# Performance work log

Hardware: AMD Instinct MI355X
Metric: run time of the kernel (lower is better)

Reference implementation:

```python
import jax, jax.numpy as jnp
import numpy as np

D_MODEL = 1024
N_HEADS = 16
FEATURE_DIM = 16
HEAD_DIM = D_MODEL // N_HEADS  # 64
EPS = 1e-12


def taylor_exp(x):
    """2nd-order Taylor feature map of exp(q^T k / sqrt(d)).
    x: (b, h, l, d) -> (b, h, l, 1 + d + d^2)"""
    d = x.shape[-1]
    rd = jnp.sqrt(jnp.asarray(d, x.dtype))      # sqrt(d)
    rrd = jnp.sqrt(rd)                          # d^(1/4)
    r2 = jnp.sqrt(jnp.asarray(2.0, x.dtype))
    x2 = (x[..., :, None] * x[..., None, :]).reshape(*x.shape[:-1], d * d) / r2
    ones = jnp.ones_like(x[..., :1])
    return jnp.concatenate([ones, x / rrd, x2 / rd], axis=-1)


def setup_inputs() -> dict:
    key = jax.random.key(0)
    k0, k1, k2, k3, k4 = jax.random.split(key, 5)
    b, l = 1, 1024
    scale = 1.0 / np.sqrt(D_MODEL)
    hidden_states = jax.random.normal(k0, (b, l, D_MODEL), dtype=jnp.float32)
    Wq = jax.random.normal(k1, (N_HEADS * FEATURE_DIM, D_MODEL), dtype=jnp.float32) * scale
    Wk = jax.random.normal(k2, (N_HEADS * FEATURE_DIM, D_MODEL), dtype=jnp.float32) * scale
    Wv = jax.random.normal(k3, (N_HEADS * HEAD_DIM, D_MODEL), dtype=jnp.float32) * scale
    Wo = jax.random.normal(k4, (D_MODEL, N_HEADS * HEAD_DIM), dtype=jnp.float32) * scale
    return {"hidden_states": hidden_states, "Wq": Wq, "Wk": Wk, "Wv": Wv, "Wo": Wo}


def reference(hidden_states, Wq, Wk, Wv, Wo):
    b, l, _ = hidden_states.shape
    # projections (bias-free)
    q = (hidden_states @ Wq.T).reshape(b, l, N_HEADS, FEATURE_DIM).transpose(0, 2, 1, 3)
    k = (hidden_states @ Wk.T).reshape(b, l, N_HEADS, FEATURE_DIM).transpose(0, 2, 1, 3)
    v = (hidden_states @ Wv.T).reshape(b, l, N_HEADS, HEAD_DIM).transpose(0, 2, 1, 3)
    qf = taylor_exp(q)   # (b, h, l, D) with D = 1 + d + d^2 = 273
    kf = taylor_exp(k)
    # causal linear attention via associative KV accumulation
    # kv_state[l] = sum_{t<=l} phi(k_t) outer v_t  -> (b, h, l, head_dim, D)
    kv_state = jnp.cumsum(kf[..., None, :] * v[..., :, None], axis=2)
    num = jnp.einsum('bhlD,bhldD->bhld', qf, kv_state)
    den = jnp.einsum('bhlD,bhlD->bhl', qf, jnp.cumsum(kf, axis=2))[..., None] + EPS
    y = num / den                                # (b, h, l, head_dim)
    y = y.transpose(0, 2, 1, 3).reshape(b, l, N_HEADS * HEAD_DIM)
    return y @ Wo.T
```

## Files before the change

### kernel.cpp

```cpp
#include <hip/hip_runtime.h>

#define LSEQ 1024
#define DMODEL 1024
#define NHEADS 16
#define FDIM 16
#define HDIM 64
#define CHUNK 64
#define NCHUNK 16

typedef __attribute__((ext_vector_type(8))) short short8;
typedef __attribute__((ext_vector_type(4))) float floatx4;

__device__ __forceinline__ unsigned short f2bf(float f) {
    return __builtin_bit_cast(unsigned short, (__bf16)f);
}

__device__ __forceinline__ int block_detect_fp32(const unsigned short* wq) {
    __shared__ int cnt;
    if (threadIdx.x == 0) cnt = 0;
    __syncthreads();
    int bad = 0;
    for (int i = threadIdx.x; i < 1024; i += blockDim.x) {
        int e = (wq[i] >> 7) & 0xFF;
        if (e >= 143 || (e > 0 && e <= 80)) bad++;
    }
    if (bad) atomicAdd(&cnt, bad);
    __syncthreads();
    return cnt > 128;
}

#define U_QB   0
#define U_KB   262144
#define U_VT   524288
#define U_END  2621440

#define MFMA(a, b, c) __builtin_amdgcn_mfma_f32_16x16x32_bf16((a), (b), (c), 0, 0, 0)

__device__ __forceinline__ void gemm64_body(
    unsigned short (&As)[64][136], unsigned short (&Bs)[64][136],
    const void* Araw, int a_fp32, int arow0,
    const void* Braw, int b_fp32, int brow0, floatx4 acc[4]) {
    int t = threadIdx.x;
    int r = t >> 2, c0 = (t & 3) * 32;
    int wave = t >> 6, lane = t & 63;
    int ml = lane & 15, q4 = lane >> 4;
    int mq = (wave >> 1) * 32, nq = (wave & 1) * 32;
    #pragma unroll
    for (int i = 0; i < 4; ++i) acc[i] = (floatx4){0.f, 0.f, 0.f, 0.f};

    short8 av[4], bv[4], av2[4], bv2[4];
    auto cvt8 = [](float4 f0, float4 f1) {
        short8 x;
        x[0] = (short)f2bf(f0.x); x[1] = (short)f2bf(f0.y);
        x[2] = (short)f2bf(f0.z); x[3] = (short)f2bf(f0.w);
        x[4] = (short)f2bf(f1.x); x[5] = (short)f2bf(f1.y);
        x[6] = (short)f2bf(f1.z); x[7] = (short)f2bf(f1.w);
        return x;
    };
    auto stage = [&](int k0, short8* a, short8* b) {
        if (!a_fp32) {
            const unsigned short* Ap = (const unsigned short*)Araw + (size_t)(arow0 + r) * DMODEL + k0 + c0;
            #pragma unroll
            for (int j = 0; j < 4; ++j) a[j] = *(const short8*)(Ap + j * 8);
        } else {
            const float* Ap = (const float*)Araw + (size_t)(arow0 + r) * DMODEL + k0 + c0;
            #pragma unroll
            for (int j = 0; j < 4; ++j)
                a[j] = cvt8(*(const float4*)(Ap + j * 8), *(const float4*)(Ap + j * 8 + 4));
        }
        if (!b_fp32) {
            const unsigned short* Bp = (const unsigned short*)Braw + (size_t)(brow0 + r) * DMODEL + k0 + c0;
            #pragma unroll
            for (int j = 0; j < 4; ++j) b[j] = *(const short8*)(Bp + j * 8);
        } else {
            const float* Bp = (const float*)Braw + (size_t)(brow0 + r) * DMODEL + k0 + c0;
            #pragma unroll
            for (int j = 0; j < 4; ++j)
                b[j] = cvt8(*(const float4*)(Bp + j * 8), *(const float4*)(Bp + j * 8 + 4));
        }
    };

    stage(0, av, bv);
    for (int k0 = 0; k0 < DMODEL; k0 += 128) {
        __syncthreads();
        #pragma unroll
        for (int j = 0; j < 4; ++j) {
            *(short8*)&As[r][c0 + j * 8] = av[j];
            *(short8*)&Bs[r][c0 + j * 8] = bv[j];
        }
        __syncthreads();
        if (k0 + 128 < DMODEL) stage(k0 + 128, av2, bv2);
        #pragma unroll
        for (int kk = 0; kk < 4; ++kk) {
            short8 a0 = *(const short8*)&As[mq + ml][kk * 32 + q4 * 8];
            short8 a1 = *(const short8*)&As[mq + 16 + ml][kk * 32 + q4 * 8];
            short8 b0 = *(const short8*)&Bs[nq + ml][kk * 32 + q4 * 8];
            short8 b1 = *(const short8*)&Bs[nq + 16 + ml][kk * 32 + q4 * 8];
            acc[0] = MFMA(a0, b0, acc[0]); acc[1] = MFMA(a0, b1, acc[1]);
            acc[2] = MFMA(a1, b0, acc[2]); acc[3] = MFMA(a1, b1, acc[3]);
        }
        #pragma unroll
        for (int j = 0; j < 4; ++j) { av[j] = av2[j]; bv[j] = bv2[j]; }
    }
}

__global__ __launch_bounds__(256) void qkv_gemm(
    const void* __restrict__ hidR, const void* __restrict__ WqR,
    const void* __restrict__ WkR, const void* __restrict__ WvR,
    unsigned short* __restrict__ qb, unsigned short* __restrict__ kb,
    unsigned short* __restrict__ vt) {
    int fp32 = block_detect_fp32((const unsigned short*)WqR);
    __shared__ __align__(16) unsigned short As[64][136];
    __shared__ __align__(16) unsigned short Bs[64][136];
    int nb = blockIdx.x, mb = blockIdx.y;
    const void* Braw; unsigned short* Cout; int ldc, col0, br0, isv;
    if (nb < 4)      { Braw = WqR; br0 = nb * 64;       Cout = qb; ldc = 256;  col0 = nb * 64;       isv = 0; }
    else if (nb < 8) { Braw = WkR; br0 = (nb - 4) * 64; Cout = kb; ldc = 256;  col0 = (nb - 4) * 64; isv = 0; }
    else             { Braw = WvR; br0 = (nb - 8) * 64; Cout = vt; ldc = 0;    col0 = (nb - 8) * 64; isv = 1; }

    floatx4 acc[4];
    gemm64_body(As, Bs, hidR, fp32, mb * 64, Braw, fp32, br0, acc);

    int wave = threadIdx.x >> 6, lane = threadIdx.x & 63;
    int ml = lane & 15, q4 = lane >> 4;
    int mq = (wave >> 1) * 32, nq = (wave & 1) * 32;
    if (!isv) {
        #pragma unroll
        for (int mi = 0; mi < 2; ++mi)
            #pragma unroll
            for (int ni = 0; ni < 2; ++ni) {
                floatx4 a = acc[mi * 2 + ni];
                int nloc = nq + ni * 16 + ml;
                #pragma unroll
                for (int r4 = 0; r4 < 4; ++r4) {
                    int row = mb * 64 + mq + mi * 16 + q4 * 4 + r4;
                    Cout[(size_t)row * ldc + col0 + nloc] = f2bf(a[r4]);
                }
            }
    } else {
        #pragma unroll
        for (int mi = 0; mi < 2; ++mi)
            #pragma unroll
            for (int ni = 0; ni < 2; ++ni) {
                floatx4 a = acc[mi * 2 + ni];
                int n = col0 + nq + ni * 16 + ml;
                int row0 = mb * 64 + mq + mi * 16 + q4 * 4;
                ushort4 o;
                o.x = f2bf(a[0]); o.y = f2bf(a[1]);
                o.z = f2bf(a[2]); o.w = f2bf(a[3]);
                *(ushort4*)&vt[(size_t)n * 1024 + row0] = o;
            }
    }
}

__global__ __launch_bounds__(256) void flash_partial(
    const unsigned short* __restrict__ qb, const unsigned short* __restrict__ kb,
    const unsigned short* __restrict__ vt,
    float* __restrict__ numW, float* __restrict__ denW) {
    int idx = blockIdx.x & 255;
    int s = blockIdx.x >> 8;
    int h = idx & 15, c = idx >> 4;
    int half = (c + 1) >> 1;
    int j0 = s ? half : 0;
    int j1 = s ? c : half - 1;
    int l0 = c * CHUNK;
    __shared__ __align__(16) unsigned short qs[64][40];
    __shared__ __align__(16) unsigned short ksm[64][40];
    __shared__ __align__(16) unsigned short vT[80][72];
    __shared__ __align__(16) unsigned short P[64][72];
    int t = threadIdx.x, lane = t & 63, wave = t >> 6;
    int ml = lane & 15, q4 = lane >> 4;
    int m0 = wave * 16;
    int sm = t >> 2, si4 = (t & 3) * 4, sc16 = (t & 3) * 16;

    {
        *(ushort4*)&qs[sm][si4] = *(const ushort4*)&qb[(size_t)(l0 + sm) * 256 + h * 16 + si4];
        ushort4 z = {0, 0, 0, 0};
        *(ushort4*)&qs[sm][16 + si4]  = z;
        *(ushort4*)&ksm[sm][16 + si4] = z;
    }
    if (t < 64) {
        vT[64][t] = 0x3F80;
        #pragma unroll
        for (int i = 65; i < 80; ++i) vT[i][t] = 0;
    }

    auto load_kv = [&](int j, ushort4& kr, short8& v0, short8& v1) {
        kr = *(const ushort4*)&kb[(size_t)(j * 64 + sm) * 256 + h * 16 + si4];
        const unsigned short* vp = vt + (size_t)(h * 64 + sm) * 1024 + j * 64 + sc16;
        v0 = *(const short8*)vp;
        v1 = *(const short8*)(vp + 8);
    };

    floatx4 acc[5];
    #pragma unroll
    for (int i = 0; i < 5; ++i) acc[i] = (floatx4){0.f, 0.f, 0.f, 0.f};

    ushort4 kr, kr2; short8 va, vb2, va2, vb22;
    if (j0 <= j1) {
        load_kv(j0, kr, va, vb2);
        for (int j = j0; j <= j1; ++j) {
            *(ushort4*)&ksm[sm][si4] = kr;
            *(short8*)&vT[sm][sc16]     = va;
            *(short8*)&vT[sm][sc16 + 8] = vb2;
            __syncthreads();
            if (j < j1) load_kv(j + 1, kr2, va2, vb22);

            short8 aq = *(const short8*)&qs[m0 + ml][q4 * 8];
            bool diag = (j == c);
            #pragma unroll
            for (int nt = 0; nt < 4; ++nt) {
                short8 bk = *(const short8*)&ksm[nt * 16 + ml][q4 * 8];
                floatx4 s4 = {0.f, 0.f, 0.f, 0.f};
                s4 = MFMA(aq, bk, s4);
                int tt = nt * 16 + ml;
                #pragma unroll
                for (int r = 0; r < 4; ++r) {
                    int lrow = m0 + q4 * 4 + r;
                    float sc = s4[r];
                    float p = 1.f + 0.25f * sc + 0.03125f * sc * sc;
                    if (diag && tt > lrow) p = 0.f;
                    P[lrow][tt] = f2bf(p);
                }
            }

            #pragma unroll
            for (int k0 = 0; k0 < 64; k0 += 32) {
                short8 ap = *(const short8*)&P[m0 + ml][k0 + q4 * 8];
                #pragma unroll
                for (int nt = 0; nt < 5; ++nt) {
                    short8 av = *(const short8*)&vT[nt * 16 + ml][k0 + q4 * 8];
                    acc[nt] = MFMA(av, ap, acc[nt]);
                }
            }
            __syncthreads();
            kr = kr2; va = va2; vb2 = vb22;
        }
    }

    float* np = numW + ((size_t)idx * 2 + s) * 4096 + (m0 + ml) * 64;
    #pragma unroll
    for (int nt = 0; nt < 4; ++nt)
        *(floatx4*)&np[nt * 16 + q4 * 4] = acc[nt];
    if (lane < 16) denW[((size_t)idx * 2 + s) * 64 + m0 + lane] = acc[4][0];
}

__global__ __launch_bounds__(256) void out_gemm(
    const float* __restrict__ numW, const float* __restrict__ denW,
    const void* __restrict__ WoR, void* __restrict__ outv,
    const unsigned short* __restrict__ wqraw) {
    int fp32 = block_detect_fp32(wqraw);
    __shared__ __align__(16) unsigned short As[64][136];
    __shared__ __align__(16) unsigned short Bs[64][136];
    int nb = blockIdx.x, mb = blockIdx.y;
    int t = threadIdx.x;
    int r = t >> 2, c0 = (t & 3) * 32;
    int wave = t >> 6, lane = t & 63;
    int ml = lane & 15, q4 = lane >> 4;
    int mq = (wave >> 1) * 32, nq = (wave & 1) * 32;
    floatx4 acc[4];
    #pragma unroll
    for (int i = 0; i < 4; ++i) acc[i] = (floatx4){0.f, 0.f, 0.f, 0.f};

    short8 av[4], bv[4], av2[4], bv2[4];
    auto cvt8 = [](float4 f0, float4 f1) {
        short8 x;
        x[0] = (short)f2bf(f0.x); x[1] = (short)f2bf(f0.y);
        x[2] = (short)f2bf(f0.z); x[3] = (short)f2bf(f0.w);
        x[4] = (short)f2bf(f1.x); x[5] = (short)f2bf(f1.y);
        x[6] = (short)f2bf(f1.z); x[7] = (short)f2bf(f1.w);
        return x;
    };
    auto stageA = [&](int k0, short8* a) {
        int kbase = k0 + c0;
        int h = kbase >> 6;
        size_t idx = (size_t)(mb * 16 + h);
        const float* n0 = numW + idx * 2 * 4096 + r * 64 + (kbase & 63);
        const float* n1 = n0 + 4096;
        float den = denW[idx * 128 + r] + denW[idx * 128 + 64 + r] + 1e-12f;
        float dinv = 1.f / den;
        #pragma unroll
        for (int j = 0; j < 4; ++j) {
            float4 f0 = *(const float4*)(n0 + j * 8);
            float4 f1 = *(const float4*)(n0 + j * 8 + 4);
            float4 g0 = *(const float4*)(n1 + j * 8);
            float4 g1 = *(const float4*)(n1 + j * 8 + 4);
            float4 s0, s1;
            s0.x = (f0.x + g0.x) * dinv; s0.y = (f0.y + g0.y) * dinv;
            s0.z = (f0.z + g0.z) * dinv; s0.w = (f0.w + g0.w) * dinv;
            s1.x = (f1.x + g1.x) * dinv; s1.y = (f1.y + g1.y) * dinv;
            s1.z = (f1.z + g1.z) * dinv; s1.w = (f1.w + g1.w) * dinv;
            a[j] = cvt8(s0, s1);
        }
    };
    auto stageB = [&](int k0, short8* b) {
        if (!fp32) {
            const unsigned short* Bp = (const unsigned short*)WoR + (size_t)(nb * 64 + r) * DMODEL + k0 + c0;
            #pragma unroll
            for (int j = 0; j < 4; ++j) b[j] = *(const short8*)(Bp + j * 8);
        } else {
            const float* Bp = (const float*)WoR + (size_t)(nb * 64 + r) * DMODEL + k0 + c0;
            #pragma unroll
            for (int j = 0; j < 4; ++j)
                b[j] = cvt8(*(const float4*)(Bp + j * 8), *(const float4*)(Bp + j * 8 + 4));
        }
    };

    stageA(0, av); stageB(0, bv);
    for (int k0 = 0; k0 < DMODEL; k0 += 128) {
        __syncthreads();
        #pragma unroll
        for (int j = 0; j < 4; ++j) {
            *(short8*)&As[r][c0 + j * 8] = av[j];
            *(short8*)&Bs[r][c0 + j * 8] = bv[j];
        }
        __syncthreads();
        if (k0 + 128 < DMODEL) { stageA(k0 + 128, av2); stageB(k0 + 128, bv2); }
        #pragma unroll
        for (int kk = 0; kk < 4; ++kk) {
            short8 a0 = *(const short8*)&As[mq + ml][kk * 32 + q4 * 8];
            short8 a1 = *(const short8*)&As[mq + 16 + ml][kk * 32 + q4 * 8];
            short8 b0 = *(const short8*)&Bs[nq + ml][kk * 32 + q4 * 8];
            short8 b1 = *(const short8*)&Bs[nq + 16 + ml][kk * 32 + q4 * 8];
            acc[0] = MFMA(a0, b0, acc[0]); acc[1] = MFMA(a0, b1, acc[1]);
            acc[2] = MFMA(a1, b0, acc[2]); acc[3] = MFMA(a1, b1, acc[3]);
        }
        #pragma unroll
        for (int j = 0; j < 4; ++j) { av[j] = av2[j]; bv[j] = bv2[j]; }
    }

    #pragma unroll
    for (int mi = 0; mi < 2; ++mi)
        #pragma unroll
        for (int ni = 0; ni < 2; ++ni) {
            floatx4 a = acc[mi * 2 + ni];
            int n = nb * 64 + nq + ni * 16 + ml;
            #pragma unroll
            for (int r4 = 0; r4 < 4; ++r4) {
                int row = mb * 64 + mq + mi * 16 + q4 * 4 + r4;
                size_t oidx = (size_t)row * 1024 + n;
                if (fp32) ((float*)outv)[oidx] = a[r4];
                else      ((unsigned short*)outv)[oidx] = f2bf(a[r4]);
            }
        }
}

extern "C" void kernel_launch(void* const* d_in, const int* in_sizes, int n_in,
                              void* d_out, int out_size, void* d_ws, size_t ws_size,
                              hipStream_t stream) {
    unsigned short* us = (unsigned short*)d_ws;
    unsigned short* qbB = us + U_QB;
    unsigned short* kbB = us + U_KB;
    unsigned short* vtB = us + U_VT;
    float* fws  = (float*)(us + U_END);
    float* numW = fws;
    float* denW = fws + 2097152;
    size_t need = (size_t)U_END * 2ull + (size_t)(2097152 + 32768) * 4ull;
    if (ws_size < need) return;

    qkv_gemm<<<dim3(24, 16), 256, 0, stream>>>(d_in[0], d_in[1], d_in[2], d_in[3], qbB, kbB, vtB);
    flash_partial<<<dim3(512), 256, 0, stream>>>(qbB, kbB, vtB, numW, denW);
    out_gemm<<<dim3(16, 16), 256, 0, stream>>>(numW, denW, d_in[4], d_out, (const unsigned short*)d_in[1]);
}
```

Measured before the change: 148.2 us.

## Split causal attention over four key ranges and add separate combine kernel

The flash_partial kernel now splits each query chunk's key range into four parts instead of two, launching 1024 blocks to spread the triangular work more evenly across CUs. A new attn_combine kernel sums the four partials, normalizes by the denominator and writes bf16 y, so out_gemm reuses the generic gemm64_body instead of reducing partials inline. The score MFMA operands are also swapped so each lane writes a packed ushort4 to the P tile rather than scalar stores. This adds an extra kernel launch and doubles the partial-result workspace traffic.

```diff
diff --git a/kernel.cpp b/kernel.cpp
--- a/kernel.cpp
+++ b/kernel.cpp
@@ -7,6 +7,7 @@
 #define HDIM 64
 #define CHUNK 64
 #define NCHUNK 16
+#define NSPLIT 4
 
 typedef __attribute__((ext_vector_type(8))) short short8;
 typedef __attribute__((ext_vector_type(4))) float floatx4;
@@ -32,6 +33,7 @@
 #define U_QB   0
 #define U_KB   262144
 #define U_VT   524288
+#define U_YB   1572864
 #define U_END  2621440
 
 #define MFMA(a, b, c) __builtin_amdgcn_mfma_f32_16x16x32_bf16((a), (b), (c), 0, 0, 0)
@@ -160,9 +162,9 @@
     int idx = blockIdx.x & 255;
     int s = blockIdx.x >> 8;
     int h = idx & 15, c = idx >> 4;
-    int half = (c + 1) >> 1;
-    int j0 = s ? half : 0;
-    int j1 = s ? c : half - 1;
+    int n = c + 1;
+    int j0 = (n * s) >> 2;
+    int j1 = ((n * (s + 1)) >> 2) - 1;
     int l0 = c * CHUNK;
     __shared__ __align__(16) unsigned short qs[64][40];
     __shared__ __align__(16) unsigned short ksm[64][40];
@@ -208,20 +210,22 @@
 
             short8 aq = *(const short8*)&qs[m0 + ml][q4 * 8];
             bool diag = (j == c);
+            int qloc = m0 + ml;
             #pragma unroll
             for (int nt = 0; nt < 4; ++nt) {
                 short8 bk = *(const short8*)&ksm[nt * 16 + ml][q4 * 8];
                 floatx4 s4 = {0.f, 0.f, 0.f, 0.f};
-                s4 = MFMA(aq, bk, s4);
-                int tt = nt * 16 + ml;
+                s4 = MFMA(bk, aq, s4);
+                ushort4 pw;
                 #pragma unroll
                 for (int r = 0; r < 4; ++r) {
-                    int lrow = m0 + q4 * 4 + r;
+                    int tloc = nt * 16 + q4 * 4 + r;
                     float sc = s4[r];
                     float p = 1.f + 0.25f * sc + 0.03125f * sc * sc;
-                    if (diag && tt > lrow) p = 0.f;
-                    P[lrow][tt] = f2bf(p);
+                    if (diag && tloc > qloc) p = 0.f;
+                    ((unsigned short*)&pw)[r] = f2bf(p);
                 }
+                *(ushort4*)&P[qloc][nt * 16 + q4 * 4] = pw;
             }
 
             #pragma unroll
@@ -238,107 +242,71 @@
         }
     }
 
-    float* np = numW + ((size_t)idx * 2 + s) * 4096 + (m0 + ml) * 64;
+    float* np = numW + ((size_t)idx * NSPLIT + s) * 4096 + (m0 + ml) * 64;
     #pragma unroll
     for (int nt = 0; nt < 4; ++nt)
         *(floatx4*)&np[nt * 16 + q4 * 4] = acc[nt];
-    if (lane < 16) denW[((size_t)idx * 2 + s) * 64 + m0 + lane] = acc[4][0];
+    if (lane < 16) denW[((size_t)idx * NSPLIT + s) * 64 + m0 + lane] = acc[4][0];
+}
+
+__global__ __launch_bounds__(256) void attn_combine(
+    const float* __restrict__ numW, const float* __restrict__ denW,
+    unsigned short* __restrict__ ybB) {
+    int idx = blockIdx.x;
+    int h = idx & 15, c = idx >> 4;
+    int l0 = c * CHUNK;
+    int t = threadIdx.x;
+    int row = t >> 2, col0 = (t & 3) * 16;
+    const float* nb_ = numW + (size_t)idx * NSPLIT * 4096 + row * 64 + col0;
+    const float* db_ = denW + (size_t)idx * NSPLIT * 64 + row;
+    float den = db_[0] + db_[64] + db_[128] + db_[192] + 1e-12f;
+    float dinv = 1.f / den;
+    float sum[16];
+    #pragma unroll
+    for (int u = 0; u < 16; u += 4) {
+        float4 a0 = *(const float4*)(nb_ + u);
+        float4 a1 = *(const float4*)(nb_ + 4096 + u);
+        float4 a2 = *(const float4*)(nb_ + 8192 + u);
+        float4 a3 = *(const float4*)(nb_ + 12288 + u);
+        sum[u + 0] = a0.x + a1.x + a2.x + a3.x;
+        sum[u + 1] = a0.y + a1.y + a2.y + a3.y;
+        sum[u + 2] = a0.z + a1.z + a2.z + a3.z;
+        sum[u + 3] = a0.w + a1.w + a2.w + a3.w;
+    }
+    short8 o0, o1;
+    #pragma unroll
+    for (int u = 0; u < 8; ++u)  o0[u] = (short)f2bf(sum[u] * dinv);
+    #pragma unroll
+    for (int u = 0; u < 8; ++u)  o1[u] = (short)f2bf(sum[u + 8] * dinv);
+    unsigned short* yp = ybB + (size_t)(l0 + row) * 1024 + h * 64 + col0;
+    *(short8*)yp       = o0;
+    *(short8*)(yp + 8) = o1;
 }
 
 __global__ __launch_bounds__(256) void out_gemm(
-    const float* __restrict__ numW, const float* __restrict__ denW,
-    const void* __restrict__ WoR, void* __restrict__ outv,
-    const unsigned short* __restrict__ wqraw) {
+    const unsigned short* __restrict__ A, const void* __restrict__ WoR,
+    void* __restrict__ outv, const unsigned short* __restrict__ wqraw) {
     int fp32 = block_detect_fp32(wqraw);
     __shared__ __align__(16) unsigned short As[64][136];
     __shared__ __align__(16) unsigned short Bs[64][136];
     int nb = blockIdx.x, mb = blockIdx.y;
-    int t = threadIdx.x;
-    int r = t >> 2, c0 = (t & 3) * 32;
-    int wave = t >> 6, lane = t & 63;
+
+    floatx4 acc[4];
+    gemm64_body(As, Bs, A, 0, mb * 64, WoR, fp32, nb * 64, acc);
+
+    int wave = threadIdx.x >> 6, lane = threadIdx.x & 63;
     int ml = lane & 15, q4 = lane >> 4;
     int mq = (wave >> 1) * 32, nq = (wave & 1) * 32;
-    floatx4 acc[4];
-    #pragma unroll
-    for (int i = 0; i < 4; ++i) acc[i] = (floatx4){0.f, 0.f, 0.f, 0.f};
-
-    short8 av[4], bv[4], av2[4], bv2[4];
-    auto cvt8 = [](float4 f0, float4 f1) {
-        short8 x;
-        x[0] = (short)f2bf(f0.x); x[1] = (short)f2bf(f0.y);
-        x[2] = (short)f2bf(f0.z); x[3] = (short)f2bf(f0.w);
-        x[4] = (short)f2bf(f1.x); x[5] = (short)f2bf(f1.y);
-        x[6] = (short)f2bf(f1.z); x[7] = (short)f2bf(f1.w);
-        return x;
-    };
-    auto stageA = [&](int k0, short8* a) {
-        int kbase = k0 + c0;
-        int h = kbase >> 6;
-        size_t idx = (size_t)(mb * 16 + h);
-        const float* n0 = numW + idx * 2 * 4096 + r * 64 + (kbase & 63);
-        const float* n1 = n0 + 4096;
-        float den = denW[idx * 128 + r] + denW[idx * 128 + 64 + r] + 1e-12f;
-        float dinv = 1.f / den;
-        #pragma unroll
-        for (int j = 0; j < 4; ++j) {
-            float4 f0 = *(const float4*)(n0 + j * 8);
-            float4 f1 = *(const float4*)(n0 + j * 8 + 4);
-            float4 g0 = *(const float4*)(n1 + j * 8);
-            float4 g1 = *(const float4*)(n1 + j * 8 + 4);
-            float4 s0, s1;
-            s0.x = (f0.x + g0.x) * dinv; s0.y = (f0.y + g0.y) * dinv;
-            s0.z = (f0.z + g0.z) * dinv; s0.w = (f0.w + g0.w) * dinv;
-            s1.x = (f1.x + g1.x) * dinv; s1.y = (f1.y + g1.y) * dinv;
-            s1.z = (f1.z + g1.z) * dinv; s1.w = (f1.w + g1.w) * dinv;
-            a[j] = cvt8(s0, s1);
-        }
-    };
-    auto stageB = [&](int k0, short8* b) {
-        if (!fp32) {
-            const unsigned short* Bp = (const unsigned short*)WoR + (size_t)(nb * 64 + r) * DMODEL + k0 + c0;
-            #pragma unroll
-            for (int j = 0; j < 4; ++j) b[j] = *(const short8*)(Bp + j * 8);
-        } else {
-            const float* Bp = (const float*)WoR + (size_t)(nb * 64 + r) * DMODEL + k0 + c0;
-            #pragma unroll
-            for (int j = 0; j < 4; ++j)
-                b[j] = cvt8(*(const float4*)(Bp + j * 8), *(const float4*)(Bp + j * 8 + 4));
-        }
-    };
-
-    stageA(0, av); stageB(0, bv);
-    for (int k0 = 0; k0 < DMODEL; k0 += 128) {
-        __syncthreads();
-        #pragma unroll
-        for (int j = 0; j < 4; ++j) {
-            *(short8*)&As[r][c0 + j * 8] = av[j];
-            *(short8*)&Bs[r][c0 + j * 8] = bv[j];
-        }
-        __syncthreads();
-        if (k0 + 128 < DMODEL) { stageA(k0 + 128, av2); stageB(k0 + 128, bv2); }
-        #pragma unroll
-        for (int kk = 0; kk < 4; ++kk) {
-            short8 a0 = *(const short8*)&As[mq + ml][kk * 32 + q4 * 8];
-            short8 a1 = *(const short8*)&As[mq + 16 + ml][kk * 32 + q4 * 8];
-            short8 b0 = *(const short8*)&Bs[nq + ml][kk * 32 + q4 * 8];
-            short8 b1 = *(const short8*)&Bs[nq + 16 + ml][kk * 32 + q4 * 8];
-            acc[0] = MFMA(a0, b0, acc[0]); acc[1] = MFMA(a0, b1, acc[1]);
-            acc[2] = MFMA(a1, b0, acc[2]); acc[3] = MFMA(a1, b1, acc[3]);
-        }
-        #pragma unroll
-        for (int j = 0; j < 4; ++j) { av[j] = av2[j]; bv[j] = bv2[j]; }
-    }
-
     #pragma unroll
     for (int mi = 0; mi < 2; ++mi)
         #pragma unroll
         for (int ni = 0; ni < 2; ++ni) {
             floatx4 a = acc[mi * 2 + ni];
-            int n = nb * 64 + nq + ni * 16 + ml;
+            int nn = nb * 64 + nq + ni * 16 + ml;
             #pragma unroll
             for (int r4 = 0; r4 < 4; ++r4) {
                 int row = mb * 64 + mq + mi * 16 + q4 * 4 + r4;
-                size_t oidx = (size_t)row * 1024 + n;
+                size_t oidx = (size_t)row * 1024 + nn;
                 if (fp32) ((float*)outv)[oidx] = a[r4];
                 else      ((unsigned short*)outv)[oidx] = f2bf(a[r4]);
             }
@@ -352,13 +320,15 @@
     unsigned short* qbB = us + U_QB;
     unsigned short* kbB = us + U_KB;
     unsigned short* vtB = us + U_VT;
+    unsigned short* ybB = us + U_YB;
     float* fws  = (float*)(us + U_END);
     float* numW = fws;
-    float* denW = fws + 2097152;
-    size_t need = (size_t)U_END * 2ull + (size_t)(2097152 + 32768) * 4ull;
+    float* denW = fws + 4194304;
+    size_t need = (size_t)U_END * 2ull + (size_t)(4194304 + 65536) * 4ull;
     if (ws_size < need) return;
 
     qkv_gemm<<<dim3(24, 16), 256, 0, stream>>>(d_in[0], d_in[1], d_in[2], d_in[3], qbB, kbB, vtB);
-    flash_partial<<<dim3(512), 256, 0, stream>>>(qbB, kbB, vtB, numW, denW);
-    out_gemm<<<dim3(16, 16), 256, 0, stream>>>(numW, denW, d_in[4], d_out, (const unsigned short*)d_in[1]);
-}
+    flash_partial<<<dim3(1024), 256, 0, stream>>>(qbB, kbB, vtB, numW, denW);
+    attn_combine<<<dim3(256), 256, 0, stream>>>(numW, denW, ybB);
+    out_gemm<<<dim3(16, 16), 256, 0, stream>>>(ybB, d_in[4], d_out, (const unsigned short*)d_in[1]);
+}
```

After: 137.6 us. 7.1% less time.
